# Performance work log

Hardware: AMD Instinct MI355X
Metric: run time of the kernel (lower is better)

The kernel has to match this reference:

```python
import jax, jax.numpy as jnp
import numpy as np

EMBED_DIM = 1024
NUM_HEADS = 16
HEAD_DIM = EMBED_DIM // NUM_HEADS
SCALE = HEAD_DIM ** -0.5


def setup_inputs() -> dict:
    key = jax.random.key(0)
    k1, k2, k3, k4, k5, k6 = jax.random.split(key, 6)
    B, Tq, Tk = 2, 2048, 2048
    std = EMBED_DIM ** -0.5
    return {
        "x_q": jax.random.normal(k1, (B, Tq, EMBED_DIM), jnp.float32),
        "x_kv": jax.random.normal(k2, (B, Tk, EMBED_DIM), jnp.float32),
        "w_q": jax.random.normal(k3, (EMBED_DIM, EMBED_DIM), jnp.float32) * std,
        "w_kv": jax.random.normal(k4, (EMBED_DIM, 2 * EMBED_DIM), jnp.float32) * std,
        "w_proj": jax.random.normal(k5, (EMBED_DIM, EMBED_DIM), jnp.float32) * std,
        "w_rel": jax.random.normal(k6, (1, NUM_HEADS), jnp.float32) * 0.02,
    }


def reference(x_q, x_kv, w_q, w_kv, w_proj, w_rel):
    B, Tq, _ = x_q.shape
    Tk = x_kv.shape[1]
    # projections
    q = x_q @ w_q                       # [B,Tq,E]
    kv = x_kv @ w_kv                    # [B,Tk,2E]
    k, v = jnp.split(kv, 2, axis=-1)

    def heads(y, T):
        return y.reshape(B, T, NUM_HEADS, HEAD_DIM).transpose(0, 2, 1, 3)

    q = heads(q, Tq)                    # [B,H,Tq,D]
    k = heads(k, Tk)
    v = heads(v, Tk)

    logits = jnp.einsum('bhqd,bhkd->bhqk', q, k) * SCALE  # [B,H,Tq,Tk]

    # relative position bias: Dense(1 -> H) applied to (pos_q - pos_k)
    rel = jnp.arange(Tq, dtype=jnp.float32)[:, None] - jnp.arange(Tk, dtype=jnp.float32)[None, :]
    bias = rel[..., None] * w_rel[0]                      # [Tq,Tk,H]
    bias = bias.transpose(2, 0, 1)[None]                  # [1,H,Tq,Tk]
    logits = logits + bias

    attn = jax.nn.softmax(logits, axis=-1)                # dropout=0 / inference -> identity
    out = jnp.einsum('bhqk,bhkd->bhqd', attn, v)          # [B,H,Tq,D]
    out = out.transpose(0, 2, 1, 3).reshape(B, Tq, EMBED_DIM)
    return out @ w_proj
```

## Files before the change

kernel.cpp:

```cpp
#include <hip/hip_runtime.h>

typedef __attribute__((ext_vector_type(8))) short short8;
typedef __attribute__((ext_vector_type(8))) __bf16 bf16x8;
typedef __attribute__((ext_vector_type(4))) float f32x4;
typedef __attribute__((ext_vector_type(8))) unsigned short ushort8v;
typedef __attribute__((ext_vector_type(4))) unsigned short ushort4v;

#define NB 2
#define TQ 2048
#define TKK 2048
#define EMB 1024
#define NH 16
#define HD 64

__device__ __forceinline__ unsigned short f2bf(float f){
  union { float f; unsigned u; } v; v.f = f;
  unsigned r = v.u + 0x7FFFu + ((v.u >> 16) & 1u);
  return (unsigned short)(r >> 16);
}
__device__ __forceinline__ unsigned short f2bfr(float f){
  union { float f; unsigned u; } v; v.f = f;
  return (unsigned short)((v.u + 0x8000u) >> 16);
}

#define GLOAD_LDS16(g, l) __builtin_amdgcn_global_load_lds( \
    (const __attribute__((address_space(1))) void*)(g), \
    (__attribute__((address_space(3))) void*)(l), 16, 0, 0)

#define SWZ(row, inner) ((inner) ^ (((row)&7)<<4))

__device__ __forceinline__ void mfma16(const short8& a, const short8& b, f32x4& c){
  c = __builtin_amdgcn_mfma_f32_16x16x32_bf16(
        __builtin_bit_cast(bf16x8, a), __builtin_bit_cast(bf16x8, b), c, 0, 0, 0);
}

__global__ __launch_bounds__(256) void cvt_f32_bf16(const float* __restrict__ in,
    unsigned short* __restrict__ out, int n4){
  int i = blockIdx.x*256 + threadIdx.x;
  if (i >= n4) return;
  float4 v = ((const float4*)in)[i];
  ushort4v o;
  o.x = f2bf(v.x); o.y = f2bf(v.y); o.z = f2bf(v.z); o.w = f2bf(v.w);
  ((ushort4v*)out)[i] = o;
}

__global__ __launch_bounds__(256) void wt_transpose(const float* __restrict__ W,
    unsigned short* __restrict__ WT, int K, int N){
  __shared__ unsigned short tile[64][72];
  int k0 = blockIdx.y*64, n0 = blockIdx.x*64;
  int tid = threadIdx.x;
  #pragma unroll
  for (int it=0; it<4; ++it){
    int c = tid + it*256;
    int r = c>>4, c4 = (c&15)*4;
    float4 v = *(const float4*)(W + (long)(k0+r)*N + n0 + c4);
    tile[r][c4+0]=f2bf(v.x); tile[r][c4+1]=f2bf(v.y);
    tile[r][c4+2]=f2bf(v.z); tile[r][c4+3]=f2bf(v.w);
  }
  __syncthreads();
  #pragma unroll
  for (int it=0; it<2; ++it){
    int c = tid + it*256;
    int n = c>>3, k8 = (c&7)*8;
    ushort8v o;
    #pragma unroll
    for (int j=0;j<8;++j) o[j] = tile[k8+j][n];
    *(ushort8v*)(WT + (long)(n0+n)*K + k0 + k8) = o;
  }
}

__global__ __launch_bounds__(256) void v_transpose(const unsigned short* __restrict__ KV,
    unsigned short* __restrict__ VT){
  __shared__ unsigned short tile[64][72];
  int bh = blockIdx.y; int b = bh>>4, h = bh&15;
  int t0 = blockIdx.x*64;
  int tid = threadIdx.x;
  #pragma unroll
  for (int it=0; it<2; ++it){
    int c = tid + it*256;
    int r = c>>3, d8 = (c&7)*8;
    ushort8v v = *(const ushort8v*)(KV + (long)(b*TKK + t0 + r)*(2*EMB) + EMB + h*HD + d8);
    #pragma unroll
    for (int j=0;j<8;++j) tile[r][d8+j] = v[j];
  }
  __syncthreads();
  #pragma unroll
  for (int it=0; it<2; ++it){
    int c = tid + it*256;
    int d = c>>3, t8 = (c&7)*8;
    ushort8v o;
    #pragma unroll
    for (int j=0;j<8;++j) o[j] = tile[t8+j][d];
    *(ushort8v*)(VT + (long)(bh*HD + d)*TKK + t0 + t8) = o;
  }
}

template<int OUT_BF16>
__global__ __launch_bounds__(256,2) void gemm_bt(const unsigned short* __restrict__ A,
    const unsigned short* __restrict__ BT, void* __restrict__ Cout,
    int M, int N, int K){
  __shared__ unsigned short Al[128*64];
  __shared__ unsigned short Bl[128*64];
  const int tid = threadIdx.x;
  const int wave = tid>>6, lane = tid&63;
  const int m0 = blockIdx.y*128, n0 = blockIdx.x*128;
  const int wm = (wave>>1)*64, wn = (wave&1)*64;
  const int g = lane>>4, lr = lane&15;
  const int srow = lane>>3;
  const int sinner = (lane&7)*16;
  f32x4 acc[4][4] = {};

  for (int k0=0; k0<K; k0+=64){
    #pragma unroll
    for (int j=0;j<4;++j){
      int chunk = wave*4 + j;
      int row = chunk*8 + srow;
      int kb = SWZ(row, sinner);
      GLOAD_LDS16(A + (long)(m0+row)*K + k0 + (kb>>1), Al + chunk*512);
      GLOAD_LDS16(BT + (long)(n0+row)*K + k0 + (kb>>1), Bl + chunk*512);
    }
    __syncthreads();
    #pragma unroll
    for (int kk=0;kk<2;++kk){
      short8 af[4], bfr[4];
      const int kbyte = kk*64 + g*16;
      #pragma unroll
      for (int i=0;i<4;++i){
        int ar = wm + i*16 + lr;
        af[i] = *(const short8*)((const char*)Al + ar*128 + SWZ(ar, kbyte));
        int br = wn + i*16 + lr;
        bfr[i] = *(const short8*)((const char*)Bl + br*128 + SWZ(br, kbyte));
      }
      #pragma unroll
      for (int i=0;i<4;++i)
        #pragma unroll
        for (int jn=0;jn<4;++jn)
          mfma16(af[i], bfr[jn], acc[i][jn]);
    }
    __syncthreads();
  }
  #pragma unroll
  for (int i=0;i<4;++i){
    int row = m0 + wm + i*16 + g*4;
    #pragma unroll
    for (int jn=0;jn<4;++jn){
      int col = n0 + wn + jn*16 + lr;
      #pragma unroll
      for (int r=0;r<4;++r){
        if (OUT_BF16)
          ((unsigned short*)Cout)[(long)(row+r)*N + col] = f2bf(acc[i][jn][r]);
        else
          ((float*)Cout)[(long)(row+r)*N + col] = acc[i][jn][r];
      }
    }
  }
}

__global__ __launch_bounds__(512,4) void attn_kernel(const unsigned short* __restrict__ Qb,
    const unsigned short* __restrict__ KVb, const unsigned short* __restrict__ VT,
    const float* __restrict__ w_rel, unsigned short* __restrict__ Ob){
  __shared__ unsigned short Kl[64*64];
  __shared__ unsigned short Vl[64*64];
  __shared__ unsigned short Pl[8][16*64];
  const int bh = blockIdx.y, b = bh>>4, h = bh&15;
  const int q0 = blockIdx.x*128;
  const int tid = threadIdx.x, wave = tid>>6, lane = tid&63;
  const int g = lane>>4, lr = lane&15;
  const int srow = lane>>3, sinner = (lane&7)*16;
  const float C1 = 0.125f*1.44269504f;
  const float wr2 = w_rel[h]*1.44269504f;
  const float w64 = 64.0f*wr2;
  char* Pw = (char*)(&Pl[wave][0]);

  short8 qf[2];
  #pragma unroll
  for (int kk=0;kk<2;++kk)
    qf[kk] = *(const short8*)(Qb + (long)(b*TQ + q0 + wave*16 + lr)*EMB + h*HD + kk*32 + g*8);

  const float bq = (float)(q0 + wave*16 + lr)*wr2;
  float dl[4][4];
  #pragma unroll
  for (int n=0;n<4;++n)
    #pragma unroll
    for (int r=0;r<4;++r)
      dl[n][r] = bq - (float)(n*16 + 4*g + r)*wr2;

  short8 ones;
  #pragma unroll
  for (int j=0;j<8;++j) ones[j] = (short)0x3F80;

  f32x4 oacc[4] = {};
  f32x4 lacc = {};
  float Mx = -1e30f;

  for (int kt=0; kt<TKK; kt+=64){
    {
      int row = wave*8 + srow;
      int kb = SWZ(row, sinner);
      GLOAD_LDS16(KVb + (long)(b*TKK + kt + row)*(2*EMB) + h*HD + (kb>>1), Kl + wave*512);
      GLOAD_LDS16(VT + (long)(bh*HD + row)*TKK + kt + (kb>>1), Vl + wave*512);
    }
    __syncthreads();

    f32x4 sacc[4] = {};
    #pragma unroll
    for (int kk=0;kk<2;++kk){
      short8 kf[4];
      const int kbyte = kk*64 + g*16;
      #pragma unroll
      for (int n=0;n<4;++n){
        int trow = n*16 + lr;
        kf[n] = *(const short8*)((const char*)Kl + trow*128 + SWZ(trow, kbyte));
      }
      #pragma unroll
      for (int n=0;n<4;++n)
        mfma16(kf[n], qf[kk], sacc[n]);
    }

    #pragma unroll
    for (int n=0;n<4;++n)
      #pragma unroll
      for (int r=0;r<4;++r)
        sacc[n][r] = fmaf(sacc[n][r], C1, dl[n][r]);

    float rowmax;
    {
      float a0 = fmaxf(fmaxf(sacc[0][0],sacc[0][1]), fmaxf(sacc[0][2],sacc[0][3]));
      float a1 = fmaxf(fmaxf(sacc[1][0],sacc[1][1]), fmaxf(sacc[1][2],sacc[1][3]));
      float a2 = fmaxf(fmaxf(sacc[2][0],sacc[2][1]), fmaxf(sacc[2][2],sacc[2][3]));
      float a3 = fmaxf(fmaxf(sacc[3][0],sacc[3][1]), fmaxf(sacc[3][2],sacc[3][3]));
      rowmax = fmaxf(fmaxf(a0,a1), fmaxf(a2,a3));
      rowmax = fmaxf(rowmax, __shfl_xor(rowmax, 16, 64));
      rowmax = fmaxf(rowmax, __shfl_xor(rowmax, 32, 64));
    }

    if (__any(rowmax > Mx + 8.0f)){
      float Mn = fmaxf(Mx, rowmax);
      float rf = exp2f(Mx - Mn);
      Mx = Mn;
      float rfo[4];
      #pragma unroll
      for (int r=0;r<4;++r) rfo[r] = __shfl(rf, 4*g + r, 64);
      #pragma unroll
      for (int n=0;n<4;++n)
        #pragma unroll
        for (int r=0;r<4;++r) oacc[n][r] *= rfo[r];
      #pragma unroll
      for (int r=0;r<4;++r) lacc[r] *= rfo[r];
    }

    #pragma unroll
    for (int n=0;n<4;++n){
      ushort4v w;
      #pragma unroll
      for (int r=0;r<4;++r)
        w[r] = f2bfr(exp2f(sacc[n][r] - Mx));
      int inner = 32*n + 8*g;
      *(ushort4v*)(Pw + lr*128 + SWZ(lr, inner)) = w;
    }

    __syncthreads();

    #pragma unroll
    for (int kk=0;kk<2;++kk){
      const int kbyte = kk*64 + g*16;
      short8 pf = *(const short8*)(Pw + lr*128 + SWZ(lr, kbyte));
      #pragma unroll
      for (int n=0;n<4;++n){
        int vrow = n*16 + lr;
        short8 vf = *(const short8*)((const char*)Vl + vrow*128 + SWZ(vrow, kbyte));
        mfma16(pf, vf, oacc[n]);
      }
      mfma16(pf, ones, lacc);
    }

    #pragma unroll
    for (int n=0;n<4;++n)
      #pragma unroll
      for (int r=0;r<4;++r)
        dl[n][r] -= w64;

    __syncthreads();
  }

  #pragma unroll
  for (int r=0;r<4;++r){
    float inv = 1.0f / lacc[r];
    int q = q0 + wave*16 + 4*g + r;
    #pragma unroll
    for (int n=0;n<4;++n){
      int d = n*16 + lr;
      Ob[(long)(b*TQ + q)*EMB + h*HD + d] = f2bf(oacc[n][r]*inv);
    }
  }
}

extern "C" void kernel_launch(void* const* d_in, const int* in_sizes, int n_in,
                              void* d_out, int out_size, void* d_ws, size_t ws_size,
                              hipStream_t stream){
  const float* x_q    = (const float*)d_in[0];
  const float* x_kv   = (const float*)d_in[1];
  const float* w_q    = (const float*)d_in[2];
  const float* w_kv   = (const float*)d_in[3];
  const float* w_proj = (const float*)d_in[4];
  const float* w_rel  = (const float*)d_in[5];
  (void)in_sizes; (void)n_in; (void)out_size; (void)ws_size;
  char* ws = (char*)d_ws;
  const size_t MB = 1024*1024;
  unsigned short* Qb   = (unsigned short*)(ws + 0);
  unsigned short* KVb  = (unsigned short*)(ws + 8*MB);
  unsigned short* WpT  = (unsigned short*)(ws + 24*MB);
  unsigned short* WqT  = (unsigned short*)(ws + 26*MB);
  unsigned short* WkvT = (unsigned short*)(ws + 28*MB);
  unsigned short* Aq   = (unsigned short*)(ws + 32*MB);
  unsigned short* Akv  = (unsigned short*)(ws + 40*MB);
  unsigned short* Ob   = Aq;
  unsigned short* VTt  = Akv;
  float* out = (float*)d_out;

  cvt_f32_bf16<<<4096, 256, 0, stream>>>(x_q,  Aq,  (NB*TQ*EMB)/4);
  cvt_f32_bf16<<<4096, 256, 0, stream>>>(x_kv, Akv, (NB*TKK*EMB)/4);
  wt_transpose<<<dim3(16,16), 256, 0, stream>>>(w_q,    WqT,  EMB, EMB);
  wt_transpose<<<dim3(32,16), 256, 0, stream>>>(w_kv,   WkvT, EMB, 2*EMB);
  wt_transpose<<<dim3(16,16), 256, 0, stream>>>(w_proj, WpT,  EMB, EMB);
  gemm_bt<1><<<dim3(8,32),  256, 0, stream>>>(Aq,  WqT,  Qb,  NB*TQ, EMB,   EMB);
  gemm_bt<1><<<dim3(16,32), 256, 0, stream>>>(Akv, WkvT, KVb, NB*TKK, 2*EMB, EMB);
  v_transpose<<<dim3(32,32), 256, 0, stream>>>(KVb, VTt);
  attn_kernel<<<dim3(16,32), 512, 0, stream>>>(Qb, KVb, VTt, w_rel, Ob);
  gemm_bt<0><<<dim3(8,32),  256, 0, stream>>>(Ob, WpT, out, NB*TQ, EMB, EMB);
}
```

Before: 175.6 us.

## Merge Q and KV GEMMs, shuffle P in registers, remap attention blocks

The Q and KV projection GEMMs are merged into one launch with a 24-column grid, so the two small grids no longer run back to back. GEMM launch bounds move from 2 to 3 blocks per SM. In attention, the softmax probabilities are rearranged into MFMA A-operand layout with cross-lane shuffles instead of an LDS write, a __syncthreads and a read-back. Block IDs are also remapped so that neighbouring blocks work on different heads. The changes cut LDS traffic, one barrier per tile and a launch, at the cost of extra shuffle and select instructions and possible register pressure.

Result: slower. 190.8 us (+8.6%).

```diff
diff --git a/kernel.cpp b/kernel.cpp
--- a/kernel.cpp
+++ b/kernel.cpp
@@ -96,14 +96,12 @@
 }
 
 template<int OUT_BF16>
-__global__ __launch_bounds__(256,2) void gemm_bt(const unsigned short* __restrict__ A,
+__device__ __forceinline__ void gemm_body(const unsigned short* __restrict__ A,
     const unsigned short* __restrict__ BT, void* __restrict__ Cout,
-    int M, int N, int K){
-  __shared__ unsigned short Al[128*64];
-  __shared__ unsigned short Bl[128*64];
+    int M, int N, int K, int m0, int n0,
+    unsigned short* Al, unsigned short* Bl){
   const int tid = threadIdx.x;
   const int wave = tid>>6, lane = tid&63;
-  const int m0 = blockIdx.y*128, n0 = blockIdx.x*128;
   const int wm = (wave>>1)*64, wn = (wave&1)*64;
   const int g = lane>>4, lr = lane&15;
   const int srow = lane>>3;
@@ -156,21 +154,44 @@
   }
 }
 
+template<int OUT_BF16>
+__global__ __launch_bounds__(256,3) void gemm_bt(const unsigned short* __restrict__ A,
+    const unsigned short* __restrict__ BT, void* __restrict__ Cout,
+    int M, int N, int K){
+  __shared__ unsigned short Al[128*64];
+  __shared__ unsigned short Bl[128*64];
+  gemm_body<OUT_BF16>(A, BT, Cout, M, N, K, blockIdx.y*128, blockIdx.x*128, Al, Bl);
+}
+
+__global__ __launch_bounds__(256,3) void gemm_qkv(
+    const unsigned short* __restrict__ Aq,  const unsigned short* __restrict__ WqT,  unsigned short* __restrict__ Qb,
+    const unsigned short* __restrict__ Akv, const unsigned short* __restrict__ WkvT, unsigned short* __restrict__ KVb){
+  __shared__ unsigned short Al[128*64];
+  __shared__ unsigned short Bl[128*64];
+  const int x = blockIdx.x;
+  if (x < 8)
+    gemm_body<1>(Aq,  WqT,  Qb,  NB*TQ, EMB,   EMB, blockIdx.y*128, x*128,     Al, Bl);
+  else
+    gemm_body<1>(Akv, WkvT, KVb, NB*TKK, 2*EMB, EMB, blockIdx.y*128, (x-8)*128, Al, Bl);
+}
+
 __global__ __launch_bounds__(512,4) void attn_kernel(const unsigned short* __restrict__ Qb,
     const unsigned short* __restrict__ KVb, const unsigned short* __restrict__ VT,
     const float* __restrict__ w_rel, unsigned short* __restrict__ Ob){
   __shared__ unsigned short Kl[64*64];
   __shared__ unsigned short Vl[64*64];
-  __shared__ unsigned short Pl[8][16*64];
-  const int bh = blockIdx.y, b = bh>>4, h = bh&15;
-  const int q0 = blockIdx.x*128;
+  const int id  = blockIdx.x + 16*blockIdx.y;
+  const int nid = (id & 7)*64 + (id >> 3);
+  const int qb  = nid & 15, bh = nid >> 4;
+  const int b = bh>>4, h = bh&15;
+  const int q0 = qb*128;
   const int tid = threadIdx.x, wave = tid>>6, lane = tid&63;
   const int g = lane>>4, lr = lane&15;
+  const int a1 = g>>1, a0 = g&1;
   const int srow = lane>>3, sinner = (lane&7)*16;
   const float C1 = 0.125f*1.44269504f;
   const float wr2 = w_rel[h]*1.44269504f;
   const float w64 = 64.0f*wr2;
-  char* Pw = (char*)(&Pl[wave][0]);
 
   short8 qf[2];
   #pragma unroll
@@ -225,11 +246,11 @@
 
     float rowmax;
     {
-      float a0 = fmaxf(fmaxf(sacc[0][0],sacc[0][1]), fmaxf(sacc[0][2],sacc[0][3]));
-      float a1 = fmaxf(fmaxf(sacc[1][0],sacc[1][1]), fmaxf(sacc[1][2],sacc[1][3]));
-      float a2 = fmaxf(fmaxf(sacc[2][0],sacc[2][1]), fmaxf(sacc[2][2],sacc[2][3]));
-      float a3 = fmaxf(fmaxf(sacc[3][0],sacc[3][1]), fmaxf(sacc[3][2],sacc[3][3]));
-      rowmax = fmaxf(fmaxf(a0,a1), fmaxf(a2,a3));
+      float x0 = fmaxf(fmaxf(sacc[0][0],sacc[0][1]), fmaxf(sacc[0][2],sacc[0][3]));
+      float x1 = fmaxf(fmaxf(sacc[1][0],sacc[1][1]), fmaxf(sacc[1][2],sacc[1][3]));
+      float x2 = fmaxf(fmaxf(sacc[2][0],sacc[2][1]), fmaxf(sacc[2][2],sacc[2][3]));
+      float x3 = fmaxf(fmaxf(sacc[3][0],sacc[3][1]), fmaxf(sacc[3][2],sacc[3][3]));
+      rowmax = fmaxf(fmaxf(x0,x1), fmaxf(x2,x3));
       rowmax = fmaxf(rowmax, __shfl_xor(rowmax, 16, 64));
       rowmax = fmaxf(rowmax, __shfl_xor(rowmax, 32, 64));
     }
@@ -249,29 +270,55 @@
       for (int r=0;r<4;++r) lacc[r] *= rfo[r];
     }
 
+    unsigned pw[4][2];
     #pragma unroll
     for (int n=0;n<4;++n){
-      ushort4v w;
-      #pragma unroll
-      for (int r=0;r<4;++r)
-        w[r] = f2bfr(exp2f(sacc[n][r] - Mx));
-      int inner = 32*n + 8*g;
-      *(ushort4v*)(Pw + lr*128 + SWZ(lr, inner)) = w;
-    }
-
-    __syncthreads();
+      unsigned short e0 = f2bfr(exp2f(sacc[n][0]-Mx));
+      unsigned short e1 = f2bfr(exp2f(sacc[n][1]-Mx));
+      unsigned short e2 = f2bfr(exp2f(sacc[n][2]-Mx));
+      unsigned short e3 = f2bfr(exp2f(sacc[n][3]-Mx));
+      pw[n][0] = (unsigned)e0 | ((unsigned)e1<<16);
+      pw[n][1] = (unsigned)e2 | ((unsigned)e3<<16);
+    }
+    unsigned keepv[2][2], recvv[2][2];
+    #pragma unroll
+    for (int n1=0;n1<2;++n1)
+      #pragma unroll
+      for (int hh=0;hh<2;++hh){
+        keepv[n1][hh] = pw[2*n1 + a1][hh];
+        recvv[n1][hh] = (unsigned)__shfl_xor((int)pw[2*n1 + (a1^1)][hh], 32, 64);
+      }
+    unsigned stayv[2][2], rc2[2][2];
+    #pragma unroll
+    for (int n1=0;n1<2;++n1)
+      #pragma unroll
+      for (int hh=0;hh<2;++hh){
+        unsigned st = (a0 == a1) ? keepv[n1][hh] : recvv[n1][hh];
+        unsigned sd = (a0 == a1) ? recvv[n1][hh] : keepv[n1][hh];
+        stayv[n1][hh] = st;
+        rc2[n1][hh] = (unsigned)__shfl_xor((int)sd, 16, 64);
+      }
+    short8 pa[2];
+    #pragma unroll
+    for (int kk=0;kk<2;++kk){
+      union { unsigned u[4]; short8 s; } asmb;
+      asmb.u[0] = (a0==0) ? stayv[kk][0] : rc2[kk][0];
+      asmb.u[1] = (a0==0) ? stayv[kk][1] : rc2[kk][1];
+      asmb.u[2] = (a0==1) ? stayv[kk][0] : rc2[kk][0];
+      asmb.u[3] = (a0==1) ? stayv[kk][1] : rc2[kk][1];
+      pa[kk] = asmb.s;
+    }
 
     #pragma unroll
     for (int kk=0;kk<2;++kk){
       const int kbyte = kk*64 + g*16;
-      short8 pf = *(const short8*)(Pw + lr*128 + SWZ(lr, kbyte));
       #pragma unroll
       for (int n=0;n<4;++n){
         int vrow = n*16 + lr;
         short8 vf = *(const short8*)((const char*)Vl + vrow*128 + SWZ(vrow, kbyte));
-        mfma16(pf, vf, oacc[n]);
-      }
-      mfma16(pf, ones, lacc);
+        mfma16(pa[kk], vf, oacc[n]);
+      }
+      mfma16(pa[kk], ones, lacc);
     }
 
     #pragma unroll
@@ -323,8 +370,7 @@
   wt_transpose<<<dim3(16,16), 256, 0, stream>>>(w_q,    WqT,  EMB, EMB);
   wt_transpose<<<dim3(32,16), 256, 0, stream>>>(w_kv,   WkvT, EMB, 2*EMB);
   wt_transpose<<<dim3(16,16), 256, 0, stream>>>(w_proj, WpT,  EMB, EMB);
-  gemm_bt<1><<<dim3(8,32),  256, 0, stream>>>(Aq,  WqT,  Qb,  NB*TQ, EMB,   EMB);
-  gemm_bt<1><<<dim3(16,32), 256, 0, stream>>>(Akv, WkvT, KVb, NB*TKK, 2*EMB, EMB);
+  gemm_qkv<<<dim3(24,32), 256, 0, stream>>>(Aq, WqT, Qb, Akv, WkvT, KVb);
   v_transpose<<<dim3(32,32), 256, 0, stream>>>(KVb, VTt);
   attn_kernel<<<dim3(16,32), 512, 0, stream>>>(Qb, KVb, VTt, w_rel, Ob);
   gemm_bt<0><<<dim3(8,32),  256, 0, stream>>>(Ob, WpT, out, NB*TQ, EMB, EMB);
```
